# Performance work log

Hardware: AMD Instinct MI355X
Metric: run time of the kernel (lower is better)

Reference implementation:

```python
import jax, jax.numpy as jnp
import numpy as np

# Grid / layout constants (match init_kwargs)
NX, NY = 2048, 2048
XL, YL = 0.0, 0.0
HX = 1.0 / NX  # bin_size_x
HY = 1.0 / NY  # bin_size_y
NUM_NODES = 1_000_000
NUM_MOVABLE = 900_000


def compute_velocity_field(phi, hx, hy):
    """v = -grad(phi) via central differences, one-sided at boundaries.
    phi: [nx, ny] -> (vx, vy) each [nx, ny]."""
    vx = jnp.concatenate([
        -(phi[1:2, :] - phi[0:1, :]) / hx,          # forward diff at x=0
        -(phi[2:, :] - phi[:-2, :]) / (2.0 * hx),   # central in interior
        -(phi[-1:, :] - phi[-2:-1, :]) / hx,        # backward diff at x=nx-1
    ], axis=0)
    vy = jnp.concatenate([
        -(phi[:, 1:2] - phi[:, 0:1]) / hy,
        -(phi[:, 2:] - phi[:, :-2]) / (2.0 * hy),
        -(phi[:, -1:] - phi[:, -2:-1]) / hy,
    ], axis=1)
    return vx, vy


def setup_inputs() -> dict:
    key = jax.random.key(0)
    k1, k2 = jax.random.split(key)
    # Node positions in [0,1)x[0,1): x coords then y coords.
    pos = jax.random.uniform(k1, (2 * NUM_NODES,), dtype=jnp.float32)
    # Solved transport potential on the bin grid (stand-in for multigrid output).
    potential_field = jax.random.normal(k2, (NX, NY), dtype=jnp.float32)
    return {"pos": pos, "potential_field": potential_field}


def reference(pos, potential_field):
    # Forward of FlowBasedDensityPotentialFunction (post-solve part):
    # velocity = -grad(phi); energy = 0.5 * sum(|v|^2).
    vx, vy = compute_velocity_field(potential_field, HX, HY)
    energy = 0.5 * (jnp.sum(vx * vx) + jnp.sum(vy * vy))
    return energy
```

## Files before the change

### kernel.cpp

```cpp
#include <hip/hip_runtime.h>

#define NXG 2048
#define NYG 2048
__device__ __forceinline__ float inv_h()  { return 2048.0f; }
__device__ __forceinline__ float inv_2h() { return 1024.0f; }

#define BLOCK 256
#define GRID  1024

__global__ __launch_bounds__(BLOCK) void
energy_partial_kernel(const float* __restrict__ phi, float* __restrict__ partial) {
    const int totalChunks = (NXG * NYG) / 4;
    float acc = 0.0f;

    for (int c = blockIdx.x * blockDim.x + threadIdx.x;
         c < totalChunks;
         c += gridDim.x * blockDim.x) {
        const int i  = c >> 9;
        const int j4 = (c & 511) << 2;
        const float* row = phi + (size_t)i * NYG;

        const float4 self = *(const float4*)(row + j4);

        const int im1 = (i > 0)        ? i - 1 : 0;
        const int ip1 = (i < NXG - 1)  ? i + 1 : NXG - 1;
        const float sx = (i == 0 || i == NXG - 1) ? inv_h() : inv_2h();
        const float4 up = *(const float4*)(phi + (size_t)im1 * NYG + j4);
        const float4 dn = *(const float4*)(phi + (size_t)ip1 * NYG + j4);

        const float vx0 = (dn.x - up.x) * sx;
        const float vx1 = (dn.y - up.y) * sx;
        const float vx2 = (dn.z - up.z) * sx;
        const float vx3 = (dn.w - up.w) * sx;

        float vy0, vy1, vy2, vy3;
        if (j4 == 0) {
            vy0 = (self.y - self.x) * inv_h();
        } else {
            const float left = row[j4 - 1];
            vy0 = (self.y - left) * inv_2h();
        }
        vy1 = (self.z - self.x) * inv_2h();
        vy2 = (self.w - self.y) * inv_2h();
        if (j4 + 4 == NYG) {
            vy3 = (self.w - self.z) * inv_h();
        } else {
            const float right = row[j4 + 4];
            vy3 = (right - self.z) * inv_2h();
        }

        acc += vx0 * vx0 + vx1 * vx1 + vx2 * vx2 + vx3 * vx3
             + vy0 * vy0 + vy1 * vy1 + vy2 * vy2 + vy3 * vy3;
    }

    #pragma unroll
    for (int off = 32; off > 0; off >>= 1)
        acc += __shfl_down(acc, off, 64);

    __shared__ float smem[BLOCK / 64];
    const int lane = threadIdx.x & 63;
    const int wave = threadIdx.x >> 6;
    if (lane == 0) smem[wave] = acc;
    __syncthreads();
    if (threadIdx.x == 0) {
        float s = 0.0f;
        #pragma unroll
        for (int w = 0; w < BLOCK / 64; ++w) s += smem[w];
        partial[blockIdx.x] = s;
    }
}

__global__ __launch_bounds__(BLOCK) void
energy_finalize_kernel(const float* __restrict__ partial, float* __restrict__ out) {
    float acc = 0.0f;
    for (int idx = threadIdx.x; idx < GRID; idx += BLOCK)
        acc += partial[idx];

    #pragma unroll
    for (int off = 32; off > 0; off >>= 1)
        acc += __shfl_down(acc, off, 64);

    __shared__ float smem[BLOCK / 64];
    const int lane = threadIdx.x & 63;
    const int wave = threadIdx.x >> 6;
    if (lane == 0) smem[wave] = acc;
    __syncthreads();
    if (threadIdx.x == 0) {
        float s = 0.0f;
        #pragma unroll
        for (int w = 0; w < BLOCK / 64; ++w) s += smem[w];
        out[0] = 0.5f * s;
    }
}

extern "C" void kernel_launch(void* const* d_in, const int* in_sizes, int n_in,
                              void* d_out, int out_size, void* d_ws, size_t ws_size,
                              hipStream_t stream) {
    const float* phi = (const float*)d_in[1];
    float* out = (float*)d_out;
    float* partial = (float*)d_ws;

    energy_partial_kernel<<<GRID, BLOCK, 0, stream>>>(phi, partial);
    energy_finalize_kernel<<<1, BLOCK, 0, stream>>>(partial, out);
}
```

Measured before the change: 77.59 us.

## Process 4-row strips per thread and finalize with atomicAdd

New measurement: 83.08 us. 1.07x slower.

```diff
diff --git a/kernel.cpp b/kernel.cpp
--- a/kernel.cpp
+++ b/kernel.cpp
@@ -9,48 +9,86 @@
 #define GRID  1024
 
 __global__ __launch_bounds__(BLOCK) void
-energy_partial_kernel(const float* __restrict__ phi, float* __restrict__ partial) {
-    const int totalChunks = (NXG * NYG) / 4;
+energy_kernel(const float* __restrict__ phi, float* __restrict__ out) {
+    const int bs = ((blockIdx.x & 7) << 7) + (blockIdx.x >> 3);
+    const int c  = bs * BLOCK + threadIdx.x;
+    const int s  = c >> 9;
+    const int j4 = (c & 511) << 2;
+
+    const int i0 = 4 * s;
+    const int rm = (s > 0)   ? i0 - 1 : 0;
+    const int rp = (s < 511) ? i0 + 4 : NXG - 1;
+    const float sx0 = (s == 0)   ? inv_h() : inv_2h();
+    const float sx3 = (s == 511) ? inv_h() : inv_2h();
+
+    const float* Rm = phi + (size_t)rm * NYG;
+    const float* R0 = phi + (size_t)(i0 + 0) * NYG;
+    const float* R1 = phi + (size_t)(i0 + 1) * NYG;
+    const float* R2 = phi + (size_t)(i0 + 2) * NYG;
+    const float* R3 = phi + (size_t)(i0 + 3) * NYG;
+    const float* Rp = phi + (size_t)rp * NYG;
+
+    const float4 m  = *(const float4*)(Rm + j4);
+    const float4 r0 = *(const float4*)(R0 + j4);
+    const float4 r1 = *(const float4*)(R1 + j4);
+    const float4 r2 = *(const float4*)(R2 + j4);
+    const float4 r3 = *(const float4*)(R3 + j4);
+    const float4 p  = *(const float4*)(Rp + j4);
+
     float acc = 0.0f;
 
-    for (int c = blockIdx.x * blockDim.x + threadIdx.x;
-         c < totalChunks;
-         c += gridDim.x * blockDim.x) {
-        const int i  = c >> 9;
-        const int j4 = (c & 511) << 2;
-        const float* row = phi + (size_t)i * NYG;
+    {
+        float v;
+        v = (r1.x - m.x) * sx0; acc += v * v;
+        v = (r1.y - m.y) * sx0; acc += v * v;
+        v = (r1.z - m.z) * sx0; acc += v * v;
+        v = (r1.w - m.w) * sx0; acc += v * v;
+        v = (r2.x - r0.x) * inv_2h(); acc += v * v;
+        v = (r2.y - r0.y) * inv_2h(); acc += v * v;
+        v = (r2.z - r0.z) * inv_2h(); acc += v * v;
+        v = (r2.w - r0.w) * inv_2h(); acc += v * v;
+        v = (r3.x - r1.x) * inv_2h(); acc += v * v;
+        v = (r3.y - r1.y) * inv_2h(); acc += v * v;
+        v = (r3.z - r1.z) * inv_2h(); acc += v * v;
+        v = (r3.w - r1.w) * inv_2h(); acc += v * v;
+        v = (p.x - r2.x) * sx3; acc += v * v;
+        v = (p.y - r2.y) * sx3; acc += v * v;
+        v = (p.z - r2.z) * sx3; acc += v * v;
+        v = (p.w - r2.w) * sx3; acc += v * v;
+    }
 
-        const float4 self = *(const float4*)(row + j4);
-
-        const int im1 = (i > 0)        ? i - 1 : 0;
-        const int ip1 = (i < NXG - 1)  ? i + 1 : NXG - 1;
-        const float sx = (i == 0 || i == NXG - 1) ? inv_h() : inv_2h();
-        const float4 up = *(const float4*)(phi + (size_t)im1 * NYG + j4);
-        const float4 dn = *(const float4*)(phi + (size_t)ip1 * NYG + j4);
-
-        const float vx0 = (dn.x - up.x) * sx;
-        const float vx1 = (dn.y - up.y) * sx;
-        const float vx2 = (dn.z - up.z) * sx;
-        const float vx3 = (dn.w - up.w) * sx;
-
-        float vy0, vy1, vy2, vy3;
+    {
+        float l0, l1, l2, l3, q0, q1, q2, q3;
+        float e0, e3;
         if (j4 == 0) {
-            vy0 = (self.y - self.x) * inv_h();
+            l0 = r0.x; l1 = r1.x; l2 = r2.x; l3 = r3.x; e0 = inv_h();
         } else {
-            const float left = row[j4 - 1];
-            vy0 = (self.y - left) * inv_2h();
+            l0 = R0[j4 - 1]; l1 = R1[j4 - 1]; l2 = R2[j4 - 1]; l3 = R3[j4 - 1];
+            e0 = inv_2h();
         }
-        vy1 = (self.z - self.x) * inv_2h();
-        vy2 = (self.w - self.y) * inv_2h();
         if (j4 + 4 == NYG) {
-            vy3 = (self.w - self.z) * inv_h();
+            q0 = r0.w; q1 = r1.w; q2 = r2.w; q3 = r3.w; e3 = inv_h();
         } else {
-            const float right = row[j4 + 4];
-            vy3 = (right - self.z) * inv_2h();
+            q0 = R0[j4 + 4]; q1 = R1[j4 + 4]; q2 = R2[j4 + 4]; q3 = R3[j4 + 4];
+            e3 = inv_2h();
         }
-
-        acc += vx0 * vx0 + vx1 * vx1 + vx2 * vx2 + vx3 * vx3
-             + vy0 * vy0 + vy1 * vy1 + vy2 * vy2 + vy3 * vy3;
+        float v;
+        v = (r0.y - l0) * e0; acc += v * v;
+        v = (r1.y - l1) * e0; acc += v * v;
+        v = (r2.y - l2) * e0; acc += v * v;
+        v = (r3.y - l3) * e0; acc += v * v;
+        v = (r0.z - r0.x) * inv_2h(); acc += v * v;
+        v = (r1.z - r1.x) * inv_2h(); acc += v * v;
+        v = (r2.z - r2.x) * inv_2h(); acc += v * v;
+        v = (r3.z - r3.x) * inv_2h(); acc += v * v;
+        v = (r0.w - r0.y) * inv_2h(); acc += v * v;
+        v = (r1.w - r1.y) * inv_2h(); acc += v * v;
+        v = (r2.w - r2.y) * inv_2h(); acc += v * v;
+        v = (r3.w - r3.y) * inv_2h(); acc += v * v;
+        v = (q0 - r0.z) * e3; acc += v * v;
+        v = (q1 - r1.z) * e3; acc += v * v;
+        v = (q2 - r2.z) * e3; acc += v * v;
+        v = (q3 - r3.z) * e3; acc += v * v;
     }
 
     #pragma unroll
@@ -63,33 +101,10 @@
     if (lane == 0) smem[wave] = acc;
     __syncthreads();
     if (threadIdx.x == 0) {
-        float s = 0.0f;
+        float s4 = 0.0f;
         #pragma unroll
-        for (int w = 0; w < BLOCK / 64; ++w) s += smem[w];
-        partial[blockIdx.x] = s;
-    }
-}
-
-__global__ __launch_bounds__(BLOCK) void
-energy_finalize_kernel(const float* __restrict__ partial, float* __restrict__ out) {
-    float acc = 0.0f;
-    for (int idx = threadIdx.x; idx < GRID; idx += BLOCK)
-        acc += partial[idx];
-
-    #pragma unroll
-    for (int off = 32; off > 0; off >>= 1)
-        acc += __shfl_down(acc, off, 64);
-
-    __shared__ float smem[BLOCK / 64];
-    const int lane = threadIdx.x & 63;
-    const int wave = threadIdx.x >> 6;
-    if (lane == 0) smem[wave] = acc;
-    __syncthreads();
-    if (threadIdx.x == 0) {
-        float s = 0.0f;
-        #pragma unroll
-        for (int w = 0; w < BLOCK / 64; ++w) s += smem[w];
-        out[0] = 0.5f * s;
+        for (int w = 0; w < BLOCK / 64; ++w) s4 += smem[w];
+        atomicAdd(out, 0.5f * s4);
     }
 }
 
@@ -98,8 +113,7 @@
                               hipStream_t stream) {
     const float* phi = (const float*)d_in[1];
     float* out = (float*)d_out;
-    float* partial = (float*)d_ws;
 
-    energy_partial_kernel<<<GRID, BLOCK, 0, stream>>>(phi, partial);
-    energy_finalize_kernel<<<1, BLOCK, 0, stream>>>(partial, out);
+    hipMemsetAsync(out, 0, sizeof(float) * (size_t)out_size, stream);
+    energy_kernel<<<GRID, BLOCK, 0, stream>>>(phi, out);
 }
```
